# Optimization experiments

Hardware: AMD Instinct MI355X
Metric: run time of the kernel (lower is better)

The kernel has to match this reference:

```python
import jax, jax.numpy as jnp
import numpy as np

CROP = 3          # crop_size
MAX_CROP = 2 * CROP  # 6 -> 6x6 = 36 offsets (faithful to range(max_crop))
H = 384


def reference(predict, target, target_mask):
    # mask both images
    t = target * target_mask
    p = predict * target_mask

    B, C, _, _ = p.shape
    hw = H - MAX_CROP  # 378

    # cropped target: [:, :, 3:-3, 3:-3] -> [B, C, 378, 378]
    ct = t[:, :, CROP:-CROP, CROP:-CROP]

    def c_mse_at(u, v):
        # shifted predict window [B, C, 378, 378]
        cp = jax.lax.dynamic_slice(p, (0, 0, u, v), (B, C, hw, hw))
        bb = jnp.mean(ct - cp)           # brightness bias (scalar)
        return jnp.mean((cp + bb - ct) ** 2)  # MSE after bias correction

    offs = jnp.arange(MAX_CROP)
    uu, vv = jnp.meshgrid(offs, offs, indexing='ij')
    losses = jax.vmap(c_mse_at)(uu.ravel(), vv.ravel())  # [36]

    cMSE = jnp.min(losses)
    score = -10.0 * jnp.log10(cMSE)  # cPSNR
    return score


def setup_inputs() -> dict:
    key = jax.random.key(0)
    k1, k2, k3 = jax.random.split(key, 3)
    shape = (32, 1, 384, 384)
    predict = jax.random.uniform(k1, shape, dtype=jnp.float32)
    target = jax.random.uniform(k2, shape, dtype=jnp.float32)
    target_mask = jax.random.uniform(k3, shape, dtype=jnp.float32)
    return {"predict": predict, "target": target, "target_mask": target_mask}
```

## Files before the change

kernel.cpp:

```cpp
#include <hip/hip_runtime.h>
#include <hip/hip_bf16.h>
#include <math.h>


#define NIMG 32
#define IMGSZ (384 * 384)
#define NRT 126
#define NSG 48
#define BSZ 768
#define NCC 252
#define NEDGE 64
#define SWZD 256
#define SCH 32
#define NM 40
#define MSTRIDE 252
#define MQUADS 63
#define NE 262

__global__ __launch_bounds__(BSZ) void probav_fused_kernel(
    const float* __restrict__ predict,
    const float* __restrict__ target,
    const float* __restrict__ mask,
    float* __restrict__ mpart ,
    double* __restrict__ epart ) {

  const int t = threadIdx.x;
  const int lane = t & 63;
  const int w = t >> 6;

  if (blockIdx.x >= NEDGE) {
    const int sb = blockIdx.x - NEDGE;
    const int cb = (sb & 7) * SCH + (sb >> 3);
    if (cb >= NCC) return;

    __shared__ float red[12 * NM];

    const int tid = cb * BSZ + t;
    const int img = tid / (NRT * NSG);
    const int rem = tid - img * (NRT * NSG);
    const int rt  = rem / NSG;
    const int sg  = rem - rt * NSG;
    const int r0  = rt * 3;
    const int jb  = sg * 8;
    const size_t base = (size_t)img * IMGSZ;
    const bool isLastRt = (rt == NRT - 1);

    float ct[3][8];
    float t1 = 0.f, t2 = 0.f;
#pragma unroll
    for (int rr = 0; rr < 3; ++rr) {
      const float4* tq = reinterpret_cast<const float4*>(target + base + (size_t)(r0 + rr + 3) * 384 + jb);
      const float4* mq = reinterpret_cast<const float4*>(mask   + base + (size_t)(r0 + rr + 3) * 384 + jb);
      float tv[12], mv[12];
#pragma unroll
      for (int q = 0; q < 3; ++q) {
        float4 a = tq[q];
        float4 b = mq[q];
        tv[4 * q + 0] = a.x; tv[4 * q + 1] = a.y; tv[4 * q + 2] = a.z; tv[4 * q + 3] = a.w;
        mv[4 * q + 0] = b.x; mv[4 * q + 1] = b.y; mv[4 * q + 2] = b.z; mv[4 * q + 3] = b.w;
      }
#pragma unroll
      for (int x = 0; x < 8; ++x) {
        float v = tv[3 + x] * mv[3 + x];
        v = (jb + x < 378) ? v : 0.f;
        ct[rr][x] = v;
        t1 += v;
        t2 = fmaf(v, v, t2);
      }
    }

    float cc[36];
#pragma unroll
    for (int o = 0; o < 36; ++o) cc[o] = 0.f;
    float tot1 = 0.f, tot2 = 0.f;
    const int ownR = isLastRt ? 8 : 3;

#pragma unroll
    for (int R = 0; R < 8; ++R) {
      const float4* pq = reinterpret_cast<const float4*>(predict + base + (size_t)(r0 + R) * 384 + jb);
      const float4* mq = reinterpret_cast<const float4*>(mask    + base + (size_t)(r0 + R) * 384 + jb);
      float pm[16];
#pragma unroll
      for (int q = 0; q < 4; ++q) {
        float4 a = pq[q];
        float4 b = mq[q];
        pm[4 * q + 0] = a.x * b.x;
        pm[4 * q + 1] = a.y * b.y;
        pm[4 * q + 2] = a.z * b.z;
        pm[4 * q + 3] = a.w * b.w;
      }
      if (R < ownR) {
#pragma unroll
        for (int x = 0; x < 8; ++x) {
          tot1 += pm[x];
          tot2 = fmaf(pm[x], pm[x], tot2);
        }
      }
      const int rlo = (R > 5) ? (R - 5) : 0;
      const int rhi = (R < 2) ? R : 2;
#pragma unroll
      for (int rr = rlo; rr <= rhi; ++rr) {
        const int u = R - rr;
#pragma unroll
        for (int v = 0; v < 6; ++v) {
#pragma unroll
          for (int x = 0; x < 8; ++x) {
            cc[u * 6 + v] = fmaf(ct[rr][x], pm[v + x], cc[u * 6 + v]);
          }
        }
      }
    }

#pragma unroll
    for (int o = 0; o < 36; ++o) {
      float a = cc[o];
#pragma unroll
      for (int off = 32; off > 0; off >>= 1) a += __shfl_down(a, off);
      if (lane == 0) red[w * NM + o] = a;
    }
    {
      float a = t1, b = t2, c = tot1, d = tot2;
#pragma unroll
      for (int off = 32; off > 0; off >>= 1) {
        a += __shfl_down(a, off);
        b += __shfl_down(b, off);
        c += __shfl_down(c, off);
        d += __shfl_down(d, off);
      }
      if (lane == 0) { red[w * NM + 36] = a; red[w * NM + 37] = b; red[w * NM + 38] = c; red[w * NM + 39] = d; }
    }
    __syncthreads();
    if (t < NM) {
      float v = 0.f;
#pragma unroll
      for (int k = 0; k < 12; ++k) v += red[k * NM + t];
      mpart[t * MSTRIDE + cb] = v;
    }
  } else {
    const int img = blockIdx.x >> 1;
    const int slice = blockIdx.x & 1;
    const size_t base = (size_t)img * IMGSZ;

    if (slice == 0) {
      if (w < 10) {
        const int ridx = w;
        const int row = (ridx < 5) ? ridx : (373 + ridx);
        const float* pr = predict + base + (size_t)row * 384;
        const float* mr = mask    + base + (size_t)row * 384;
        double e1 = 0.0, e2 = 0.0;
#pragma unroll
        for (int k = 0; k < 6; ++k) {
          float v = pr[lane + 64 * k] * mr[lane + 64 * k];
          e1 += v;
          e2 += (double)v * v;
        }
#pragma unroll
        for (int off = 32; off > 0; off >>= 1) {
          e1 += __shfl_down(e1, off);
          e2 += __shfl_down(e2, off);
        }
        if (lane == 0) {
          epart[(size_t)ridx        * NIMG + img] = e1;
          epart[(size_t)(10 + ridx) * NIMG + img] = e2;
        }
      }
      if (t >= 640 && t < 750) {
        const int k = t - 640;
        const int ridx = k / 11, cidx = k % 11;
        const int row = (ridx < 5) ? ridx : (373 + ridx);
        const int col = (cidx < 5) ? cidx : (373 + cidx);
        float v = predict[base + (size_t)row * 384 + col] * mask[base + (size_t)row * 384 + col];
        epart[(size_t)(42 + k)  * NIMG + img] = (double)v;
        epart[(size_t)(152 + k) * NIMG + img] = (double)v * v;
      }
    } else {
      if (w < 11) {
        const int cidx = w;
        const int col = (cidx < 5) ? cidx : (373 + cidx);
        double f1 = 0.0, f2 = 0.0;
#pragma unroll
        for (int k = 0; k < 6; ++k) {
          const int r = lane + 64 * k;
          if (r < 383) {
            float v = predict[base + (size_t)r * 384 + col] * mask[base + (size_t)r * 384 + col];
            f1 += v;
            f2 += (double)v * v;
          }
        }
#pragma unroll
        for (int off = 32; off > 0; off >>= 1) {
          f1 += __shfl_down(f1, off);
          f2 += __shfl_down(f2, off);
        }
        if (lane == 0) {
          epart[(size_t)(20 + cidx) * NIMG + img] = f1;
          epart[(size_t)(31 + cidx) * NIMG + img] = f2;
        }
      }
    }
  }
}

__global__ void probav_final_kernel(const float* __restrict__ mpart,
                                    const double* __restrict__ epart,
                                    float* __restrict__ out) {
  __shared__ double M[NM];
  __shared__ double E[NE];
  __shared__ double Etmp[524];
  __shared__ double loss[36];
  const int t = threadIdx.x;
  const int lane = t & 63;
  const int w = t >> 6;

  for (int v = w; v < NM; v += 16) {
    const float4* qp = reinterpret_cast<const float4*>(mpart + v * MSTRIDE);
    double s = 0.0;
    for (int i = lane; i < MQUADS; i += 64) {
      float4 q = qp[i];
      s += (double)q.x + (double)q.y + (double)q.z + (double)q.w;
    }
#pragma unroll
    for (int off = 32; off > 0; off >>= 1) s += __shfl_down(s, off);
    if (lane == 0) M[v] = s;
  }
  if (t < 524) {
    const int e = t >> 1, si = t & 1;
    double s = 0.0;
    for (int i = si * 16; i < si * 16 + 16; ++i) s += epart[(size_t)e * NIMG + i];
    Etmp[t] = s;
  }
  __syncthreads();
  if (t < NE) E[t] = Etmp[2 * t] + Etmp[2 * t + 1];
  __syncthreads();

  if (t < 36) {
    const int u = t / 6, v = t % 6;
    double br1 = 0, br2 = 0, bc1 = 0, bc2 = 0, x1 = 0, x2 = 0;
    int rset[5], nr = 0;
    for (int j = 0; j < u; ++j) rset[nr++] = j;
    for (int j = 5 + u; j < 10; ++j) rset[nr++] = j;
    int cset[6], nc = 0;
    for (int j = 0; j < v; ++j) cset[nc++] = j;
    for (int j = 5 + v; j < 11; ++j) cset[nc++] = j;
    for (int a = 0; a < nr; ++a) { br1 += E[rset[a]]; br2 += E[10 + rset[a]]; }
    for (int b = 0; b < nc; ++b) { bc1 += E[20 + cset[b]]; bc2 += E[31 + cset[b]]; }
    for (int a = 0; a < nr; ++a)
      for (int b = 0; b < nc; ++b) {
        x1 += E[42 + rset[a] * 11 + cset[b]];
        x2 += E[152 + rset[a] * 11 + cset[b]];
      }
    const double T1 = M[36], T2 = M[37];
    const double W1 = M[38] - br1 - bc1 + x1;
    const double W2 = M[39] - br2 - bc2 + x2;
    const double CCv = M[t];
    const double N = 32.0 * 378.0 * 378.0;
    const double S1 = T1 - W1;
    const double S2 = T2 - 2.0 * CCv + W2;
    loss[t] = S2 / N - (S1 / N) * (S1 / N);
  }
  __syncthreads();
  if (t == 0) {
    double best = loss[0];
    for (int o = 1; o < 36; ++o) best = fmin(best, loss[o]);
    out[0] = (float)(-10.0 * log10(best));
  }
}

extern "C" void kernel_launch(void* const* d_in, const int* in_sizes, int n_in,
                              void* d_out, int out_size, void* d_ws, size_t ws_size,
                              hipStream_t stream) {
  const float* predict = (const float*)d_in[0];
  const float* target  = (const float*)d_in[1];
  const float* mask    = (const float*)d_in[2];
  float* out = (float*)d_out;

  float*  mpart = (float*)d_ws;
  double* epart = (double*)((char*)d_ws + NM * MSTRIDE * 4);

  probav_fused_kernel<<<NEDGE + SWZD, BSZ, 0, stream>>>(predict, target, mask, mpart, epart);
  probav_final_kernel<<<1, 1024, 0, stream>>>(mpart, epart, out);
}
```

Before: 60.87 us.

## Stage predict/mask slabs in LDS via async global_load_lds with 32-row tiles

Restructures the main correlation blocks into 256-thread blocks, each covering a 32-row by 64-column tile. Each block asynchronously copies a 37-row slab of predict and mask into swizzled shared memory with global_load_lds. Each thread then owns one target row and reads its six shifted rows from LDS, instead of having every thread reload eight overlapping rows from global memory. This cuts redundant global traffic and raises the block count, at the cost of more partial sums for the final kernel and larger LDS use per block.

```diff
diff --git a/kernel.cpp b/kernel.cpp
--- a/kernel.cpp
+++ b/kernel.cpp
@@ -5,25 +5,32 @@
 
 #define NIMG 32
 #define IMGSZ (384 * 384)
-#define NRT 126
-#define NSG 48
-#define BSZ 768
-#define NCC 252
+#define RB 32
+#define NRB 12
+#define NCB 6
+#define NCC (NIMG * NRB * NCB)
 #define NEDGE 64
-#define SWZD 256
-#define SCH 32
+#define SCH 288
 #define NM 40
-#define MSTRIDE 252
-#define MQUADS 63
+#define MSTRIDE 2304
+#define MQUADS 576
 #define NE 262
-
-__global__ __launch_bounds__(BSZ) void probav_fused_kernel(
+#define SLABR 37
+#define GRAN 24
+#define NCHUNK 14
+#define NGRP (NCHUNK * 64)
+
+__global__ __launch_bounds__(256) void probav_fused_kernel(
     const float* __restrict__ predict,
     const float* __restrict__ target,
     const float* __restrict__ mask,
     float* __restrict__ mpart ,
     double* __restrict__ epart ) {
 
+  __shared__ float Pl[NGRP * 4];
+  __shared__ float Ml[NGRP * 4];
+  __shared__ float red[4 * NM];
+
   const int t = threadIdx.x;
   const int lane = t & 63;
   const int w = t >> 6;
@@ -31,82 +38,100 @@
   if (blockIdx.x >= NEDGE) {
     const int sb = blockIdx.x - NEDGE;
     const int cb = (sb & 7) * SCH + (sb >> 3);
-    if (cb >= NCC) return;
-
-    __shared__ float red[12 * NM];
-
-    const int tid = cb * BSZ + t;
-    const int img = tid / (NRT * NSG);
-    const int rem = tid - img * (NRT * NSG);
-    const int rt  = rem / NSG;
-    const int sg  = rem - rt * NSG;
-    const int r0  = rt * 3;
-    const int jb  = sg * 8;
+    const int img = cb / (NRB * NCB);
+    const int rem = cb - img * (NRB * NCB);
+    const int rb  = rem / NCB;
+    const int jcb = rem - rb * NCB;
+    const int r0  = rb * RB;
+    const int jb0 = jcb * 64;
     const size_t base = (size_t)img * IMGSZ;
-    const bool isLastRt = (rt == NRT - 1);
-
-    float ct[3][8];
+
+    const int s   = t & 7;
+    const int rIn = t >> 3;
+    const int rr  = r0 + rIn;
+    const bool rowValid = (rr < 378);
+    const int inRow = rowValid ? (rr + 3) : 380;
+    const int jb = jb0 + 8 * s;
+    const float4* tq = reinterpret_cast<const float4*>(target + base + (size_t)inRow * 384 + jb);
+    const float4* mq = reinterpret_cast<const float4*>(mask   + base + (size_t)inRow * 384 + jb);
+    float4 tva = tq[0], tvb = tq[1], tvc = tq[2];
+    float4 mva = mq[0], mvb = mq[1], mvc = mq[2];
+
+    for (int c = w; c < NCHUNK; c += 4) {
+      const int k = c * 64 + lane;
+      int row = k / GRAN;
+      const int jl = k - row * GRAN;
+      if (row > SLABR - 1) row = SLABR - 1;
+      const int j2 = (jl & ~7) | ((jl & 7) ^ (row & 7));
+      int col = jb0 + 4 * j2; if (col > 380) col = 380;
+      int grow = r0 + row;    if (grow > 383) grow = 383;
+      const float* ps = predict + base + (size_t)grow * 384 + col;
+      const float* ms = mask    + base + (size_t)grow * 384 + col;
+      __builtin_amdgcn_global_load_lds(
+          (const __attribute__((address_space(1))) void*)ps,
+          (__attribute__((address_space(3))) void*)&Pl[c * 256], 16, 0, 0);
+      __builtin_amdgcn_global_load_lds(
+          (const __attribute__((address_space(1))) void*)ms,
+          (__attribute__((address_space(3))) void*)&Ml[c * 256], 16, 0, 0);
+    }
+
+    float ct[8];
     float t1 = 0.f, t2 = 0.f;
-#pragma unroll
-    for (int rr = 0; rr < 3; ++rr) {
-      const float4* tq = reinterpret_cast<const float4*>(target + base + (size_t)(r0 + rr + 3) * 384 + jb);
-      const float4* mq = reinterpret_cast<const float4*>(mask   + base + (size_t)(r0 + rr + 3) * 384 + jb);
+    {
       float tv[12], mv[12];
-#pragma unroll
-      for (int q = 0; q < 3; ++q) {
-        float4 a = tq[q];
-        float4 b = mq[q];
-        tv[4 * q + 0] = a.x; tv[4 * q + 1] = a.y; tv[4 * q + 2] = a.z; tv[4 * q + 3] = a.w;
-        mv[4 * q + 0] = b.x; mv[4 * q + 1] = b.y; mv[4 * q + 2] = b.z; mv[4 * q + 3] = b.w;
-      }
+      tv[0]=tva.x; tv[1]=tva.y; tv[2]=tva.z; tv[3]=tva.w;
+      tv[4]=tvb.x; tv[5]=tvb.y; tv[6]=tvb.z; tv[7]=tvb.w;
+      tv[8]=tvc.x; tv[9]=tvc.y; tv[10]=tvc.z; tv[11]=tvc.w;
+      mv[0]=mva.x; mv[1]=mva.y; mv[2]=mva.z; mv[3]=mva.w;
+      mv[4]=mvb.x; mv[5]=mvb.y; mv[6]=mvb.z; mv[7]=mvb.w;
+      mv[8]=mvc.x; mv[9]=mvc.y; mv[10]=mvc.z; mv[11]=mvc.w;
 #pragma unroll
       for (int x = 0; x < 8; ++x) {
         float v = tv[3 + x] * mv[3 + x];
-        v = (jb + x < 378) ? v : 0.f;
-        ct[rr][x] = v;
+        v = (rowValid && (jb + x < 378)) ? v : 0.f;
+        ct[x] = v;
         t1 += v;
         t2 = fmaf(v, v, t2);
       }
     }
 
+    __syncthreads();
+
     float cc[36];
 #pragma unroll
     for (int o = 0; o < 36; ++o) cc[o] = 0.f;
     float tot1 = 0.f, tot2 = 0.f;
-    const int ownR = isLastRt ? 8 : 3;
-
-#pragma unroll
-    for (int R = 0; R < 8; ++R) {
-      const float4* pq = reinterpret_cast<const float4*>(predict + base + (size_t)(r0 + R) * 384 + jb);
-      const float4* mq = reinterpret_cast<const float4*>(mask    + base + (size_t)(r0 + R) * 384 + jb);
+    const bool rowOwned = (rb < NRB - 1) || (rIn < 31);
+
+#pragma unroll
+    for (int u = 0; u < 6; ++u) {
+      const int row = rIn + u;
+      const int r8 = row & 7;
       float pm[16];
 #pragma unroll
       for (int q = 0; q < 4; ++q) {
-        float4 a = pq[q];
-        float4 b = mq[q];
-        pm[4 * q + 0] = a.x * b.x;
-        pm[4 * q + 1] = a.y * b.y;
-        pm[4 * q + 2] = a.z * b.z;
-        pm[4 * q + 3] = a.w * b.w;
-      }
-      if (R < ownR) {
+        const int jq = 2 * s + q;
+        const int js = (jq & ~7) | ((jq & 7) ^ r8);
+        const int g = row * GRAN + js;
+        float4 pv = *reinterpret_cast<const float4*>(&Pl[g * 4]);
+        float4 mv2 = *reinterpret_cast<const float4*>(&Ml[g * 4]);
+        pm[4 * q + 0] = pv.x * mv2.x;
+        pm[4 * q + 1] = pv.y * mv2.y;
+        pm[4 * q + 2] = pv.z * mv2.z;
+        pm[4 * q + 3] = pv.w * mv2.w;
+      }
+      if (u == 0 && rowOwned) {
 #pragma unroll
         for (int x = 0; x < 8; ++x) {
           tot1 += pm[x];
           tot2 = fmaf(pm[x], pm[x], tot2);
         }
       }
-      const int rlo = (R > 5) ? (R - 5) : 0;
-      const int rhi = (R < 2) ? R : 2;
-#pragma unroll
-      for (int rr = rlo; rr <= rhi; ++rr) {
-        const int u = R - rr;
-#pragma unroll
-        for (int v = 0; v < 6; ++v) {
-#pragma unroll
-          for (int x = 0; x < 8; ++x) {
-            cc[u * 6 + v] = fmaf(ct[rr][x], pm[v + x], cc[u * 6 + v]);
-          }
+#pragma unroll
+      for (int v = 0; v < 6; ++v) {
+#pragma unroll
+        for (int x = 0; x < 8; ++x) {
+          cc[u * 6 + v] = fmaf(ct[x], pm[v + x], cc[u * 6 + v]);
         }
       }
     }
@@ -131,10 +156,8 @@
     }
     __syncthreads();
     if (t < NM) {
-      float v = 0.f;
-#pragma unroll
-      for (int k = 0; k < 12; ++k) v += red[k * NM + t];
-      mpart[t * MSTRIDE + cb] = v;
+      mpart[t * MSTRIDE + cb] = red[0 * NM + t] + red[1 * NM + t] +
+                                red[2 * NM + t] + red[3 * NM + t];
     }
   } else {
     const int img = blockIdx.x >> 1;
@@ -142,8 +165,7 @@
     const size_t base = (size_t)img * IMGSZ;
 
     if (slice == 0) {
-      if (w < 10) {
-        const int ridx = w;
+      for (int ridx = w; ridx < 10; ridx += 4) {
         const int row = (ridx < 5) ? ridx : (373 + ridx);
         const float* pr = predict + base + (size_t)row * 384;
         const float* mr = mask    + base + (size_t)row * 384;
@@ -164,18 +186,16 @@
           epart[(size_t)(10 + ridx) * NIMG + img] = e2;
         }
       }
-      if (t >= 640 && t < 750) {
-        const int k = t - 640;
-        const int ridx = k / 11, cidx = k % 11;
+      if (t < 110) {
+        const int ridx = t / 11, cidx = t % 11;
         const int row = (ridx < 5) ? ridx : (373 + ridx);
         const int col = (cidx < 5) ? cidx : (373 + cidx);
         float v = predict[base + (size_t)row * 384 + col] * mask[base + (size_t)row * 384 + col];
-        epart[(size_t)(42 + k)  * NIMG + img] = (double)v;
-        epart[(size_t)(152 + k) * NIMG + img] = (double)v * v;
+        epart[(size_t)(42 + t)  * NIMG + img] = (double)v;
+        epart[(size_t)(152 + t) * NIMG + img] = (double)v * v;
       }
     } else {
-      if (w < 11) {
-        const int cidx = w;
+      for (int cidx = w; cidx < 11; cidx += 4) {
         const int col = (cidx < 5) ? cidx : (373 + cidx);
         double f1 = 0.0, f2 = 0.0;
 #pragma unroll
@@ -277,6 +297,6 @@
   float*  mpart = (float*)d_ws;
   double* epart = (double*)((char*)d_ws + NM * MSTRIDE * 4);
 
-  probav_fused_kernel<<<NEDGE + SWZD, BSZ, 0, stream>>>(predict, target, mask, mpart, epart);
+  probav_fused_kernel<<<NEDGE + NCC, 256, 0, stream>>>(predict, target, mask, mpart, epart);
   probav_final_kernel<<<1, 1024, 0, stream>>>(mpart, epart, out);
 }
```

Result: slower. 64.73 us (+6.3%).

## Process 9-row bands per thread with rolling target window and 256-thread blocks

Applied to the files above, without the earlier changes.

Each thread now covers a 9-row band instead of a 3-row strip, streaming 14 predict rows through a rolling 6-row window of masked target rows. This cuts redundant predict/mask loads (from 8 rows per 3 output rows to 14 per 9) and reduces the work-item count. Blocks shrink from 768 to 256 threads, with 316 blocks instead of 320 and a new XCD-aware block-to-chunk mapping. The cost is more registers per thread and fewer threads in total, which may hurt occupancy and latency hiding.

```diff
diff --git a/kernel.cpp b/kernel.cpp
--- a/kernel.cpp
+++ b/kernel.cpp
@@ -5,19 +5,17 @@
 
 #define NIMG 32
 #define IMGSZ (384 * 384)
-#define NRT 126
-#define NSG 48
-#define BSZ 768
+#define SEGS 48
+#define NBAND 42
+#define PERIMG (SEGS * NBAND)
 #define NCC 252
 #define NEDGE 64
-#define SWZD 256
-#define SCH 32
 #define NM 40
 #define MSTRIDE 252
 #define MQUADS 63
 #define NE 262
 
-__global__ __launch_bounds__(BSZ) void probav_fused_kernel(
+__global__ __launch_bounds__(256) void probav_fused_kernel(
     const float* __restrict__ predict,
     const float* __restrict__ target,
     const float* __restrict__ mask,
@@ -30,82 +28,80 @@
 
   if (blockIdx.x >= NEDGE) {
     const int sb = blockIdx.x - NEDGE;
-    const int cb = (sb & 7) * SCH + (sb >> 3);
-    if (cb >= NCC) return;
-
-    __shared__ float red[12 * NM];
-
-    const int tid = cb * BSZ + t;
-    const int img = tid / (NRT * NSG);
-    const int rem = tid - img * (NRT * NSG);
-    const int rt  = rem / NSG;
-    const int sg  = rem - rt * NSG;
-    const int r0  = rt * 3;
-    const int jb  = sg * 8;
+    const int xc = sb & 7, idx = sb >> 3;
+    const int cb = (xc < 4) ? (xc * 32 + idx) : (128 + (xc - 4) * 31 + idx);
+
+    __shared__ float red[4 * NM];
+
+    const int tid  = cb * 256 + t;
+    const int img  = tid / PERIMG;
+    const int rem  = tid - img * PERIMG;
+    const int band = rem / SEGS;
+    const int seg  = rem - band * SEGS;
+    const int rs   = band * 9;
+    const int jb   = seg * 8;
     const size_t base = (size_t)img * IMGSZ;
-    const bool isLastRt = (rt == NRT - 1);
-
-    float ct[3][8];
-    float t1 = 0.f, t2 = 0.f;
-#pragma unroll
-    for (int rr = 0; rr < 3; ++rr) {
-      const float4* tq = reinterpret_cast<const float4*>(target + base + (size_t)(r0 + rr + 3) * 384 + jb);
-      const float4* mq = reinterpret_cast<const float4*>(mask   + base + (size_t)(r0 + rr + 3) * 384 + jb);
-      float tv[12], mv[12];
-#pragma unroll
-      for (int q = 0; q < 3; ++q) {
-        float4 a = tq[q];
-        float4 b = mq[q];
-        tv[4 * q + 0] = a.x; tv[4 * q + 1] = a.y; tv[4 * q + 2] = a.z; tv[4 * q + 3] = a.w;
-        mv[4 * q + 0] = b.x; mv[4 * q + 1] = b.y; mv[4 * q + 2] = b.z; mv[4 * q + 3] = b.w;
-      }
-#pragma unroll
-      for (int x = 0; x < 8; ++x) {
-        float v = tv[3 + x] * mv[3 + x];
-        v = (jb + x < 378) ? v : 0.f;
-        ct[rr][x] = v;
-        t1 += v;
-        t2 = fmaf(v, v, t2);
-      }
-    }
+    const int ownK = (band == NBAND - 1) ? 14 : 9;
 
     float cc[36];
 #pragma unroll
     for (int o = 0; o < 36; ++o) cc[o] = 0.f;
-    float tot1 = 0.f, tot2 = 0.f;
-    const int ownR = isLastRt ? 8 : 3;
-
-#pragma unroll
-    for (int R = 0; R < 8; ++R) {
-      const float4* pq = reinterpret_cast<const float4*>(predict + base + (size_t)(r0 + R) * 384 + jb);
-      const float4* mq = reinterpret_cast<const float4*>(mask    + base + (size_t)(r0 + R) * 384 + jb);
+    float ctw[6][8];
+    float t1 = 0.f, t2 = 0.f, tot1 = 0.f, tot2 = 0.f;
+
+#pragma unroll
+    for (int k = 0; k < 14; ++k) {
+      if (k <= 8) {
+        const float* trow = target + base + (size_t)(rs + k + 3) * 384 + jb;
+        const float* mrow = mask   + base + (size_t)(rs + k + 3) * 384 + jb;
+        float tv[12], mv[12];
+#pragma unroll
+        for (int q = 0; q < 3; ++q) {
+          float4 a = *reinterpret_cast<const float4*>(trow + 4 * q);
+          float4 b = *reinterpret_cast<const float4*>(mrow + 4 * q);
+          tv[4 * q + 0] = a.x; tv[4 * q + 1] = a.y; tv[4 * q + 2] = a.z; tv[4 * q + 3] = a.w;
+          mv[4 * q + 0] = b.x; mv[4 * q + 1] = b.y; mv[4 * q + 2] = b.z; mv[4 * q + 3] = b.w;
+        }
+#pragma unroll
+        for (int x = 0; x < 8; ++x) {
+          float v = tv[3 + x] * mv[3 + x];
+          v = (jb + x < 378) ? v : 0.f;
+          ctw[k % 6][x] = v;
+          t1 += v;
+          t2 = fmaf(v, v, t2);
+        }
+      }
+
+      const float* prow = predict + base + (size_t)(rs + k) * 384 + jb;
+      const float* mrw2 = mask    + base + (size_t)(rs + k) * 384 + jb;
       float pm[16];
 #pragma unroll
       for (int q = 0; q < 4; ++q) {
-        float4 a = pq[q];
-        float4 b = mq[q];
+        float4 a = *reinterpret_cast<const float4*>(prow + 4 * q);
+        float4 b = *reinterpret_cast<const float4*>(mrw2 + 4 * q);
         pm[4 * q + 0] = a.x * b.x;
         pm[4 * q + 1] = a.y * b.y;
         pm[4 * q + 2] = a.z * b.z;
         pm[4 * q + 3] = a.w * b.w;
       }
-      if (R < ownR) {
+      if (k < ownK) {
 #pragma unroll
         for (int x = 0; x < 8; ++x) {
           tot1 += pm[x];
           tot2 = fmaf(pm[x], pm[x], tot2);
         }
       }
-      const int rlo = (R > 5) ? (R - 5) : 0;
-      const int rhi = (R < 2) ? R : 2;
-#pragma unroll
-      for (int rr = rlo; rr <= rhi; ++rr) {
-        const int u = R - rr;
-#pragma unroll
-        for (int v = 0; v < 6; ++v) {
-#pragma unroll
-          for (int x = 0; x < 8; ++x) {
-            cc[u * 6 + v] = fmaf(ct[rr][x], pm[v + x], cc[u * 6 + v]);
+
+#pragma unroll
+      for (int u = 0; u < 6; ++u) {
+        const int r = k - u;
+        if (r >= 0 && r <= 8) {
+#pragma unroll
+          for (int v = 0; v < 6; ++v) {
+#pragma unroll
+            for (int x = 0; x < 8; ++x) {
+              cc[u * 6 + v] = fmaf(ctw[r % 6][x], pm[v + x], cc[u * 6 + v]);
+            }
           }
         }
       }
@@ -131,10 +127,8 @@
     }
     __syncthreads();
     if (t < NM) {
-      float v = 0.f;
-#pragma unroll
-      for (int k = 0; k < 12; ++k) v += red[k * NM + t];
-      mpart[t * MSTRIDE + cb] = v;
+      mpart[t * MSTRIDE + cb] = red[0 * NM + t] + red[1 * NM + t] +
+                                red[2 * NM + t] + red[3 * NM + t];
     }
   } else {
     const int img = blockIdx.x >> 1;
@@ -142,8 +136,7 @@
     const size_t base = (size_t)img * IMGSZ;
 
     if (slice == 0) {
-      if (w < 10) {
-        const int ridx = w;
+      for (int ridx = w; ridx < 10; ridx += 4) {
         const int row = (ridx < 5) ? ridx : (373 + ridx);
         const float* pr = predict + base + (size_t)row * 384;
         const float* mr = mask    + base + (size_t)row * 384;
@@ -164,18 +157,16 @@
           epart[(size_t)(10 + ridx) * NIMG + img] = e2;
         }
       }
-      if (t >= 640 && t < 750) {
-        const int k = t - 640;
-        const int ridx = k / 11, cidx = k % 11;
+      if (t < 110) {
+        const int ridx = t / 11, cidx = t % 11;
         const int row = (ridx < 5) ? ridx : (373 + ridx);
         const int col = (cidx < 5) ? cidx : (373 + cidx);
         float v = predict[base + (size_t)row * 384 + col] * mask[base + (size_t)row * 384 + col];
-        epart[(size_t)(42 + k)  * NIMG + img] = (double)v;
-        epart[(size_t)(152 + k) * NIMG + img] = (double)v * v;
+        epart[(size_t)(42 + t)  * NIMG + img] = (double)v;
+        epart[(size_t)(152 + t) * NIMG + img] = (double)v * v;
       }
     } else {
-      if (w < 11) {
-        const int cidx = w;
+      for (int cidx = w; cidx < 11; cidx += 4) {
         const int col = (cidx < 5) ? cidx : (373 + cidx);
         double f1 = 0.0, f2 = 0.0;
 #pragma unroll
@@ -277,6 +268,6 @@
   float*  mpart = (float*)d_ws;
   double* epart = (double*)((char*)d_ws + NM * MSTRIDE * 4);
 
-  probav_fused_kernel<<<NEDGE + SWZD, BSZ, 0, stream>>>(predict, target, mask, mpart, epart);
+  probav_fused_kernel<<<NEDGE + NCC, 256, 0, stream>>>(predict, target, mask, mpart, epart);
   probav_final_kernel<<<1, 1024, 0, stream>>>(mpart, epart, out);
 }
```

Measured after the change: 49.40 us. 18.8% less time.
